# Kernel optimization log

Hardware: AMD Instinct MI355X
Metric: run time of the kernel (lower is better)

## Reference

```python
import jax, jax.numpy as jnp
import numpy as np

B, N, E, C, K, D, L, FC, IN, OUT = 2, 40000, 320000, 128, 64, 2, 4, 128, 3, 1


def _gelu(x):
    return jax.nn.gelu(x, approximate=False)  # torch F.gelu default = exact erf


def _compute_gradient(f, tgt, src, egw):
    # f: [B,C,N]; tgt,src: [B,E] int; egw: [B,E,D] -> returns [B, C*D, N]
    fT = f.transpose(0, 2, 1)  # [B,N,C]
    diff = jnp.take_along_axis(fT, src[..., None], axis=1) - jnp.take_along_axis(fT, tgt[..., None], axis=1)  # [B,E,C]
    msg = (diff[:, :, :, None] * egw[:, :, None, :]).reshape(fT.shape[0], tgt.shape[1], -1)  # [B,E,C*D], c outer / d inner
    g = jnp.zeros((fT.shape[0], fT.shape[1], msg.shape[-1]), f.dtype)
    g = g.at[jnp.arange(fT.shape[0])[:, None], tgt].add(msg)  # scatter_add over target nodes
    return g.transpose(0, 2, 1)


def _spectral(x, wc, ws, w0, bc, bs, b0, wbc, wbs, wb0):
    # x: [B,Cin,N]; wc/ws: [Cin,Cout,K]; w0: [Cin,Cout,1]; bases: [B,N,K] or [B,N,1]
    xc = jnp.einsum('bix,bxk->bik', x, wbc)
    xs = -jnp.einsum('bix,bxk->bik', x, wbs)
    x0 = jnp.einsum('bix,bxk->bik', x, wb0)
    fc = jnp.einsum('bik,iok->bok', xc, wc) - jnp.einsum('bik,iok->bok', xs, ws)
    fs = jnp.einsum('bik,iok->bok', xs, wc) + jnp.einsum('bik,iok->bok', xc, ws)
    f0 = jnp.einsum('bik,iok->bok', x0, w0)
    return (jnp.einsum('bok,bxk->box', f0, b0)
            + 2.0 * jnp.einsum('bok,bxk->box', fc, bc)
            - 2.0 * jnp.einsum('bok,bxk->box', fs, bs))


def _forward(x, node_mask, nodes, node_weights, edge_gradient_weights, modes,
             fc0_w, fc0_b, sp_wc, sp_ws, sp_w0, w_w, w_b, gw_w, gw_b,
             fc1_w, fc1_b, fc2_w, fc2_b, directed_edges):
    temp = jnp.einsum('bxd,kd->bxk', nodes, modes)
    bc = jnp.cos(temp) * node_mask
    bs = jnp.sin(temp) * node_mask
    b0 = node_mask
    wbc, wbs, wb0 = bc * node_weights, bs * node_weights, b0 * node_weights
    h = (x @ fc0_w + fc0_b).transpose(0, 2, 1)  # lift -> [B,C,N]
    tgt = directed_edges[..., 0]
    src = directed_edges[..., 1]
    nl = sp_wc.shape[0]
    for i in range(nl):
        x1 = _spectral(h, sp_wc[i], sp_ws[i], sp_w0[i], bc, bs, b0, wbc, wbs, wb0)
        x2 = jnp.einsum('oc,bcn->bon', w_w[i], h) + w_b[i][None, :, None]  # 1x1 conv
        # x3 is computed but NOT added, exactly matching the source (x = x1 + x2)
        x3 = jnp.einsum('oc,bcn->bon', gw_w[i],
                        jax.nn.soft_sign(_compute_gradient(h, tgt, src, edge_gradient_weights))) + gw_b[i][None, :, None]
        h = x1 + x2
        if i != nl - 1:
            h = _gelu(h)
    h = h.transpose(0, 2, 1)  # [B,N,C]
    h = _gelu(h @ fc1_w + fc1_b)
    return h @ fc2_w + fc2_b  # [B,N,OUT]


def setup_inputs() -> dict:
    key = jax.random.key(0)
    ks = jax.random.split(key, 16)
    scale = 1.0 / float(C * C)
    return {
        'x': jax.random.normal(ks[0], (B, N, IN), jnp.float32),
        'node_mask': jnp.ones((B, N, 1), jnp.float32),
        'nodes': jax.random.uniform(ks[1], (B, N, D), jnp.float32),
        'node_weights': jax.random.uniform(ks[2], (B, N, 1), jnp.float32) * (1.0 / N),
        'directed_edges': jax.random.randint(ks[3], (B, E, 2), 0, N, dtype=jnp.int32),
        'edge_gradient_weights': jax.random.normal(ks[4], (B, E, D), jnp.float32) * 0.1,
        'modes': jax.random.normal(ks[5], (K, D), jnp.float32) * 4.0,
        'fc0_w': jax.random.normal(ks[6], (IN, C), jnp.float32) * float(1.0 / np.sqrt(IN)),
        'fc0_b': jnp.zeros((C,), jnp.float32),
        'sp_wc': jax.random.uniform(ks[7], (L, C, C, K), jnp.float32) * scale,
        'sp_ws': jax.random.uniform(ks[8], (L, C, C, K), jnp.float32) * scale,
        'sp_w0': jax.random.uniform(ks[9], (L, C, C, 1), jnp.float32) * scale,
        'w_w': jax.random.normal(ks[10], (L, C, C), jnp.float32) * float(1.0 / np.sqrt(C)),
        'w_b': jnp.zeros((L, C), jnp.float32),
        'gw_w': jax.random.normal(ks[11], (L, C, D * C), jnp.float32) * float(1.0 / np.sqrt(D * C)),
        'gw_b': jnp.zeros((L, C), jnp.float32),
        'fc1_w': jax.random.normal(ks[12], (C, FC), jnp.float32) * float(1.0 / np.sqrt(C)),
        'fc1_b': jnp.zeros((FC,), jnp.float32),
        'fc2_w': jax.random.normal(ks[13], (FC, OUT), jnp.float32) * float(1.0 / np.sqrt(FC)),
        'fc2_b': jnp.zeros((OUT,), jnp.float32),
    }


def reference(x, node_mask, nodes, node_weights, directed_edges, edge_gradient_weights, modes,
              fc0_w, fc0_b, sp_wc, sp_ws, sp_w0, w_w, w_b, gw_w, gw_b,
              fc1_w, fc1_b, fc2_w, fc2_b):
    return _forward(x, node_mask, nodes, node_weights, edge_gradient_weights, modes,
                    fc0_w, fc0_b, sp_wc, sp_ws, sp_w0, w_w, w_b, gw_w, gw_b,
                    fc1_w, fc1_b, fc2_w, fc2_b, directed_edges)
```

## Files before the change

### kernel.cpp

```cpp
#include <hip/hip_runtime.h>
#include <math.h>

#define NN 40000
#define NP 40064
#define CC 128
#define KK 64
#define BATCH 2
#define NLAYER 4
#define FSPLITS 128
#define MODES 144
#define KTOT 256
#define NCH 626
#define NVCH 625

typedef __attribute__((ext_vector_type(8))) short bf16x8;
typedef __attribute__((ext_vector_type(4))) float f32x4;
typedef __attribute__((ext_vector_type(4))) unsigned short u16x4;
typedef __attribute__((ext_vector_type(8))) unsigned short u16x8;

__device__ __forceinline__ float gelu_exact(float x) {
    return 0.5f * x * (1.0f + erff(x * 0.70710678118654752f));
}
__device__ __forceinline__ unsigned short f2bf(float x) {
    unsigned int u = __float_as_uint(x);
    u += 0x7FFFu + ((u >> 16) & 1u);
    return (unsigned short)(u >> 16);
}
__device__ __forceinline__ float bf2f(unsigned short v) {
    return __uint_as_float(((unsigned int)v) << 16);
}

__global__ __launch_bounds__(512) void lift_fused(const float* __restrict__ x,
        const float* __restrict__ w, const float* __restrict__ bvec,
        const float* __restrict__ nodes, const float* __restrict__ mask,
        const float* __restrict__ wts, const float* __restrict__ modes,
        const float* __restrict__ fc1w, unsigned short* __restrict__ fc1t,
        unsigned short* __restrict__ Binv, float* __restrict__ maskp,
        float* __restrict__ warr, unsigned short* __restrict__ pxcs) {
    int s = blockIdx.x, b = blockIdx.y;
    int t = threadIdx.x, wv = t >> 6, l = t & 63, lo = l & 15, hi = l >> 4;
    if (b == 0 && s < 32) {
        int idx = s * 512 + t;
        int f = idx >> 7, c = idx & 127;
        fc1t[f * 128 + c] = f2bf(fc1w[c * 128 + f]);
    }
    __shared__ __align__(16) char lds[53504];
    char* Ts   = lds;
    char* Ts2  = lds + 16384;
    char* Wt   = lds + 32768;
    float* xl  = (float*)(lds + 51200);
    float* ndl = (float*)(lds + 51968);
    float* wl  = (float*)(lds + 52480);
    float* ml  = (float*)(lds + 52736);
    float* sm  = (float*)(lds + 52992);
    int c = t & 127, ng = t >> 7;
    float w0 = w[c], w1 = w[CC + c], w2 = w[2 * CC + c], bv = bvec[c];
    f32x4 accF[9];
    #pragma unroll
    for (int mt = 0; mt < 9; ++mt) accF[mt] = (f32x4){0.f, 0.f, 0.f, 0.f};
    if (t < 128) sm[t] = modes[t];
    if (t < 480) *(unsigned int*)(Wt + 129 * 128 + t * 4) = 0u;

    auto fetch = [&](int chunk) -> float {
        if (chunk >= NVCH) return 0.f;
        long base = (long)b * NN + chunk * 64;
        if (t < 192) return x[base * 3 + t];
        if (t < 320) return nodes[base * 2 + (t - 192)];
        if (t < 384) return wts[base + (t - 320)];
        if (t < 448) return mask[base + (t - 384)];
        return 0.f;
    };
    float pf = fetch(s);

    for (int chunk = s; chunk < NCH; chunk += FSPLITS) {
        int nbase = chunk * 64;
        __syncthreads();
        {
            if (t < 192)      xl[t] = pf;
            else if (t < 320) ndl[t - 192] = pf;
            else if (t < 384) wl[t - 320] = pf;
            else if (t < 448) ml[t - 384] = pf;
        }
        int nc = chunk + FSPLITS;
        if (nc < NCH) pf = fetch(nc);
        __syncthreads();
        {
            int n_ = t & 63, g = t >> 6;
            float nx = ndl[n_ * 2], ny = ndl[n_ * 2 + 1];
            float m = ml[n_];
            u16x8 cosr, sinr;
            #pragma unroll
            for (int j = 0; j < 8; ++j) {
                int k = g * 8 + j;
                float tv = nx * sm[2 * k] + ny * sm[2 * k + 1];
                float sv, cv;
                __sincosf(tv, &sv, &cv);
                unsigned short cb = f2bf(cv * m), sb = f2bf(sv * m);
                cosr[j] = cb; sinr[j] = sb;
                *(unsigned short*)(Wt + ((k * 128 + n_ * 2) ^ ((k & 7) << 4))) = cb;
                *(unsigned short*)(Wt + (((64 + k) * 128 + n_ * 2) ^ (((64 + k) & 7) << 4))) = sb;
            }
            char* brow = (char*)Binv + ((long)b * NP + nbase + n_) * 512 + g * 16;
            *(u16x8*)brow = cosr;
            *(u16x8*)(brow + 128) = sinr;
            if (t < 64) {
                *(unsigned short*)(Wt + 128 * 128 + n_ * 2) = f2bf(m);
                maskp[(long)b * NP + nbase + n_] = m;
                warr[(long)b * NP + nbase + n_] = wl[n_];
            }
        }
        {
            u16x8 hv0, hv1;
            #pragma unroll
            for (int j = 0; j < 16; ++j) {
                int n = ng * 16 + j;
                float h = bv + xl[n * 3] * w0 + xl[n * 3 + 1] * w1 + xl[n * 3 + 2] * w2;
                unsigned short hb = f2bf(h);
                unsigned short hwb = f2bf(h * wl[n]);
                if (j < 8) hv0[j] = hwb; else hv1[j - 8] = hwb;
                *(unsigned short*)(Ts + (((n << 8) + c * 2) ^ ((n & 7) << 4))) = hb;
            }
            int base2 = c * 128 + ng * 32;
            *(u16x8*)(Ts2 + (base2 ^ ((c & 7) << 4))) = hv0;
            *(u16x8*)(Ts2 + ((base2 + 16) ^ ((c & 7) << 4))) = hv1;
        }
        __syncthreads();
        char* Bdst = (char*)Binv + ((long)b * NP + nbase) * 512 + 256;
        #pragma unroll
        for (int pass = 0; pass < 2; ++pass) {
            int n = pass * 32 + (t >> 4), seg = t & 15;
            uint4 v = *(const uint4*)(Ts + (((n << 8) + (seg << 4)) ^ ((n & 7) << 4)));
            *(uint4*)(Bdst + (long)n * 512 + seg * 16) = v;
        }
        int ct = wv * 16;
        #pragma unroll
        for (int ks2 = 0; ks2 < 2; ++ks2) {
            int ar = ct + lo;
            bf16x8 a = *(const bf16x8*)(Ts2 + ((ar * 128 + ks2 * 64 + hi * 16) ^ ((ar & 7) << 4)));
            #pragma unroll
            for (int mt = 0; mt < 9; ++mt) {
                int mrow = mt * 16 + lo;
                bf16x8 bb = *(const bf16x8*)(Wt + ((mrow * 128 + ks2 * 64 + hi * 16) ^ ((mrow & 7) << 4)));
                accF[mt] = __builtin_amdgcn_mfma_f32_16x16x32_bf16(a, bb, accF[mt], 0, 0, 0);
            }
        }
    }
    unsigned short* pb = pxcs + ((long)s * BATCH + b) * CC * MODES;
    #pragma unroll
    for (int mt = 0; mt < 9; ++mt)
        #pragma unroll
        for (int r = 0; r < 4; ++r)
            pb[(long)(wv * 16 + hi * 4 + r) * MODES + mt * 16 + lo] = f2bf(accF[mt][r]);
}

__global__ __launch_bounds__(256) void reduce_kernel(const unsigned short* __restrict__ pxcs,
        float* __restrict__ xc, float* __restrict__ xs, float* __restrict__ x0) {
    int gid = blockIdx.x * 256 + threadIdx.x;
    int idx = gid >> 3, sg = gid & 7;
    float a = 0.f;
    #pragma unroll
    for (int j = 0; j < 16; ++j)
        a += bf2f(pxcs[(long)(sg * 16 + j) * (BATCH * CC * MODES) + idx]);
    a += __shfl_xor(a, 1); a += __shfl_xor(a, 2); a += __shfl_xor(a, 4);
    if (sg == 0) {
        int m = idx % MODES, bc_ = idx / MODES;
        if (m < 64)        xc[bc_ * KK + m] = a;
        else if (m < 128)  xs[bc_ * KK + m - 64] = a;
        else if (m == 128) x0[bc_] = a;
    }
}

__global__ __launch_bounds__(1024) void mix_kernel(const float* __restrict__ xc,
        const float* __restrict__ xs, const float* __restrict__ x0,
        const float* __restrict__ wc, const float* __restrict__ wsp,
        const float* __restrict__ w0, const float* __restrict__ ww,
        const float* __restrict__ wbias, unsigned short* __restrict__ A,
        float* __restrict__ f0a, float* __restrict__ wba, int layer) {
    int o = blockIdx.x, b = blockIdx.y;
    int k = threadIdx.x & 63, ig = threadIdx.x >> 6;
    const float* wcl = wc  + (long)layer * CC * CC * KK;
    const float* wsl = wsp + (long)layer * CC * CC * KK;
    float fc = 0.f, fs = 0.f;
    #pragma unroll
    for (int j = 0; j < 8; ++j) {
        int i = ig * 8 + j;
        float xci = xc[(b * CC + i) * KK + k];
        float xsi = xs[(b * CC + i) * KK + k];
        float wcv = wcl[((long)i * CC + o) * KK + k];
        float wsv = wsl[((long)i * CC + o) * KK + k];
        fc += xci * wcv + xsi * wsv;
        fs += xci * wsv - xsi * wcv;
    }
    __shared__ float rc[16][64], rs[16][64];
    rc[ig][k] = fc; rs[ig][k] = fs;
    __syncthreads();
    unsigned short* Ar = A + ((long)b * CC + o) * KTOT;
    if (ig == 0) {
        fc = 0.f; fs = 0.f;
        #pragma unroll
        for (int j = 0; j < 16; ++j) { fc += rc[j][k]; fs += rs[j][k]; }
        Ar[k]      = f2bf(2.f * fc);
        Ar[64 + k] = f2bf(-2.f * fs);
    } else if (ig == 1) {
        const float* wwl = ww + ((long)layer * CC + o) * CC;
        Ar[128 + k] = f2bf(wwl[k]);
        Ar[192 + k] = f2bf(wwl[64 + k]);
    } else if (ig == 2) {
        const float* w0l = w0 + (long)layer * CC * CC;
        float p = x0[b * CC + k] * w0l[(long)k * CC + o]
                + x0[b * CC + 64 + k] * w0l[(long)(64 + k) * CC + o];
        #pragma unroll
        for (int off = 32; off > 0; off >>= 1) p += __shfl_down(p, off, 64);
        if (k == 0) { f0a[b * CC + o] = p; wba[b * CC + o] = wbias[layer * CC + o]; }
    }
}

template <int DO_FWD, int DOGELU>
__global__ __launch_bounds__(512) void fused_inv(const unsigned short* __restrict__ Amat,
        unsigned short* Binv, const float* __restrict__ f0a, const float* __restrict__ wba,
        const float* __restrict__ maskp, const float* __restrict__ warr,
        unsigned short* __restrict__ pxcs) {
    int s = blockIdx.x, b = blockIdx.y;
    int t = threadIdx.x, wv = t >> 6, l = t & 63, lo = l & 15, hi = l >> 4;
    __shared__ __align__(16) char lds[51712];
    char* Btile = lds;
    char* Ts    = lds;
    char* Ts2   = lds + 16384;
    char* Wt    = lds + 32768;
    float* ml   = (float*)(lds + 51200);
    float* wl   = (float*)(lds + 51456);
    const unsigned short* Ab = Amat + (long)b * CC * KTOT;
    bf16x8 af[8];
    {
        const unsigned short* arow = Ab + (long)(wv * 16 + lo) * KTOT + hi * 8;
        #pragma unroll
        for (int ks = 0; ks < 8; ++ks) af[ks] = *(const bf16x8*)(arow + ks * 32);
    }
    int o0 = wv * 16 + hi * 4;
    f32x4 f0v = *(const f32x4*)(f0a + b * CC + o0);
    f32x4 wbv = *(const f32x4*)(wba + b * CC + o0);
    int swz = (lo & 7) << 4;
    f32x4 accF[9];
    #pragma unroll
    for (int mt = 0; mt < 9; ++mt) accF[mt] = (f32x4){0.f, 0.f, 0.f, 0.f};
    const char* Bbase = (const char*)Binv + (long)b * NP * 512;
    if (DO_FWD && t < 480) *(unsigned int*)(Wt + 129 * 128 + t * 4) = 0u;

    uint4 pB0 = {}, pB1 = {}, pB2 = {}, pB3 = {};
    float pmv = 0.f, pwv = 0.f;
    {
        const char* Bsrc = Bbase + (long)s * 64 * 512;
        pB0 = *(const uint4*)(Bsrc + 0 * 8192 + t * 16);
        pB1 = *(const uint4*)(Bsrc + 1 * 8192 + t * 16);
        pB2 = *(const uint4*)(Bsrc + 2 * 8192 + t * 16);
        pB3 = *(const uint4*)(Bsrc + 3 * 8192 + t * 16);
        if (t < 64) { pmv = maskp[(long)b * NP + s * 64 + t]; pwv = warr[(long)b * NP + s * 64 + t]; }
    }

    for (int chunk = s; chunk < NCH; chunk += FSPLITS) {
        int nbase = chunk * 64;
        __syncthreads();
        {
            int o = 0 * 8192 + t * 16; *(uint4*)(Btile + (o ^ (((o >> 9) & 7) << 4))) = pB0;
            o = 1 * 8192 + t * 16;     *(uint4*)(Btile + (o ^ (((o >> 9) & 7) << 4))) = pB1;
            o = 2 * 8192 + t * 16;     *(uint4*)(Btile + (o ^ (((o >> 9) & 7) << 4))) = pB2;
            o = 3 * 8192 + t * 16;     *(uint4*)(Btile + (o ^ (((o >> 9) & 7) << 4))) = pB3;
            if (t < 64) { ml[t] = pmv; wl[t] = pwv; }
        }
        int nc = chunk + FSPLITS;
        if (nc < NCH) {
            const char* Bsrc = Bbase + (long)nc * 64 * 512;
            pB0 = *(const uint4*)(Bsrc + 0 * 8192 + t * 16);
            pB1 = *(const uint4*)(Bsrc + 1 * 8192 + t * 16);
            pB2 = *(const uint4*)(Bsrc + 2 * 8192 + t * 16);
            pB3 = *(const uint4*)(Bsrc + 3 * 8192 + t * 16);
            if (t < 64) { pmv = maskp[(long)b * NP + nc * 64 + t]; pwv = warr[(long)b * NP + nc * 64 + t]; }
        }
        __syncthreads();
        if (DO_FWD) {
            int g = t >> 6, n_ = t & 63;
            int rkey = (n_ & 7) << 4;
            int raddr = n_ * 512 + g * 32;
            u16x8 r0 = *(const u16x8*)(Btile + (raddr ^ rkey));
            u16x8 r1 = *(const u16x8*)(Btile + ((raddr + 16) ^ rkey));
            #pragma unroll
            for (int i = 0; i < 8; ++i) {
                int mr = g * 16 + i;
                *(unsigned short*)(Wt + ((mr * 128 + n_ * 2) ^ ((mr & 7) << 4))) = r0[i];
            }
            #pragma unroll
            for (int i = 0; i < 8; ++i) {
                int mr = g * 16 + 8 + i;
                *(unsigned short*)(Wt + ((mr * 128 + n_ * 2) ^ ((mr & 7) << 4))) = r1[i];
            }
            if (t < 64) *(unsigned short*)(Wt + 128 * 128 + t * 2) = f2bf(ml[t]);
        }
        f32x4 acc[4];
        #pragma unroll
        for (int fn = 0; fn < 4; ++fn) acc[fn] = (f32x4){0.f, 0.f, 0.f, 0.f};
        #pragma unroll
        for (int ks = 0; ks < 8; ++ks) {
            #pragma unroll
            for (int fn = 0; fn < 4; ++fn) {
                int boff = ((fn * 16 + lo) << 9) + (ks << 6) + (hi << 4);
                bf16x8 bb = *(const bf16x8*)(Btile + (boff ^ swz));
                acc[fn] = __builtin_amdgcn_mfma_f32_16x16x32_bf16(af[ks], bb, acc[fn], 0, 0, 0);
            }
        }
        __syncthreads();
        #pragma unroll
        for (int fn = 0; fn < 4; ++fn) {
            int n = fn * 16 + lo;
            float mv = ml[n];
            u16x4 pk;
            #pragma unroll
            for (int r = 0; r < 4; ++r) {
                float v = acc[fn][r] + f0v[r] * mv + wbv[r];
                if (DOGELU) v = gelu_exact(v);
                pk[r] = f2bf(v);
                if (DO_FWD)
                    *(unsigned short*)(Ts2 + (((o0 + r) * 128 + n * 2) ^ (((o0 + r) & 7) << 4))) = f2bf(v * wl[n]);
            }
            *(u16x4*)(Ts + (((n << 8) + (o0 << 1)) ^ ((n & 7) << 4))) = pk;
        }
        __syncthreads();
        char* Bdst = (char*)Binv + ((long)b * NP + nbase) * 512 + 256;
        #pragma unroll
        for (int pass = 0; pass < 2; ++pass) {
            int n = pass * 32 + (t >> 4), seg = t & 15;
            uint4 v = *(const uint4*)(Ts + (((n << 8) + (seg << 4)) ^ ((n & 7) << 4)));
            *(uint4*)(Bdst + (long)n * 512 + seg * 16) = v;
        }
        if (DO_FWD) {
            int ct = wv * 16;
            #pragma unroll
            for (int ks2 = 0; ks2 < 2; ++ks2) {
                int ar = ct + lo;
                bf16x8 a = *(const bf16x8*)(Ts2 + ((ar * 128 + ks2 * 64 + hi * 16) ^ ((ar & 7) << 4)));
                #pragma unroll
                for (int mt = 0; mt < 9; ++mt) {
                    int mrow = mt * 16 + lo;
                    bf16x8 bb = *(const bf16x8*)(Wt + ((mrow * 128 + ks2 * 64 + hi * 16) ^ ((mrow & 7) << 4)));
                    accF[mt] = __builtin_amdgcn_mfma_f32_16x16x32_bf16(a, bb, accF[mt], 0, 0, 0);
                }
            }
        }
    }
    if (DO_FWD) {
        unsigned short* pb = pxcs + ((long)s * BATCH + b) * CC * MODES;
        #pragma unroll
        for (int mt = 0; mt < 9; ++mt)
            #pragma unroll
            for (int r = 0; r < 4; ++r)
                pb[(long)(wv * 16 + hi * 4 + r) * MODES + mt * 16 + lo] = f2bf(accF[mt][r]);
    }
}

__global__ __launch_bounds__(256) void head_mfma(const unsigned short* __restrict__ Binv,
        const unsigned short* __restrict__ fc1t, const float* __restrict__ b1,
        const float* __restrict__ fc2, const float* __restrict__ b2, float* __restrict__ out) {
    int t = threadIdx.x, wv = t >> 6, l = t & 63, lo = l & 15, hi = l >> 4;
    int b = blockIdx.y;
    int nb = (blockIdx.x * 4 + wv) * 16;
    const unsigned short* Arow = Binv + ((long)b * NP + nb + lo) * KTOT + 128 + hi * 8;
    f32x4 acc[8];
    #pragma unroll
    for (int ft = 0; ft < 8; ++ft) acc[ft] = (f32x4){0.f, 0.f, 0.f, 0.f};
    #pragma unroll
    for (int ks = 0; ks < 4; ++ks) {
        bf16x8 a = *(const bf16x8*)(Arow + ks * 32);
        #pragma unroll
        for (int ft = 0; ft < 8; ++ft) {
            bf16x8 bv = *(const bf16x8*)(fc1t + (ft * 16 + lo) * 128 + ks * 32 + hi * 8);
            acc[ft] = __builtin_amdgcn_mfma_f32_16x16x32_bf16(a, bv, acc[ft], 0, 0, 0);
        }
    }
    float s[4] = {0.f, 0.f, 0.f, 0.f};
    #pragma unroll
    for (int ft = 0; ft < 8; ++ft) {
        int f = ft * 16 + lo;
        float b1f = b1[f], f2f = fc2[f];
        #pragma unroll
        for (int r = 0; r < 4; ++r) s[r] += gelu_exact(acc[ft][r] + b1f) * f2f;
    }
    float b2v = b2[0];
    #pragma unroll
    for (int r = 0; r < 4; ++r) {
        float v = s[r];
        v += __shfl_xor(v, 1); v += __shfl_xor(v, 2);
        v += __shfl_xor(v, 4); v += __shfl_xor(v, 8);
        if (lo == 0) out[(long)b * NN + nb + hi * 4 + r] = v + b2v;
    }
}

extern "C" void kernel_launch(void* const* d_in, const int* in_sizes, int n_in,
                              void* d_out, int out_size, void* d_ws, size_t ws_size,
                              hipStream_t stream) {
    const float* x     = (const float*)d_in[0];
    const float* mask  = (const float*)d_in[1];
    const float* nodes = (const float*)d_in[2];
    const float* wts   = (const float*)d_in[3];
    const float* modes = (const float*)d_in[6];
    const float* fc0w  = (const float*)d_in[7];
    const float* fc0b  = (const float*)d_in[8];
    const float* spwc  = (const float*)d_in[9];
    const float* spws  = (const float*)d_in[10];
    const float* spw0  = (const float*)d_in[11];
    const float* ww    = (const float*)d_in[12];
    const float* wb    = (const float*)d_in[13];
    const float* fc1w  = (const float*)d_in[16];
    const float* fc1b  = (const float*)d_in[17];
    const float* fc2w  = (const float*)d_in[18];
    const float* fc2b  = (const float*)d_in[19];

    char* p = (char*)d_ws;
    auto alloc = [&](size_t bytes) { char* r = p; p += (bytes + 255) & ~255UL; return r; };
    unsigned short* Binv = (unsigned short*)alloc((size_t)BATCH * NP * KTOT * 2);
    unsigned short* Amat = (unsigned short*)alloc((size_t)BATCH * CC * KTOT * 2);
    unsigned short* fc1t = (unsigned short*)alloc((size_t)CC * 128 * 2);
    unsigned short* pxcs = (unsigned short*)alloc((size_t)FSPLITS * BATCH * CC * MODES * 2);
    float* xcb  = (float*)alloc((size_t)BATCH * CC * KK * 4);
    float* xsb  = (float*)alloc((size_t)BATCH * CC * KK * 4);
    float* x0b  = (float*)alloc((size_t)BATCH * CC * 4);
    float* f0a  = (float*)alloc((size_t)BATCH * CC * 4);
    float* wba  = (float*)alloc((size_t)BATCH * CC * 4);
    float* maskp = (float*)alloc((size_t)BATCH * NP * 4);
    float* warr  = (float*)alloc((size_t)BATCH * NP * 4);

    lift_fused<<<dim3(FSPLITS, BATCH), 512, 0, stream>>>(x, fc0w, fc0b, nodes, mask, wts,
                                                         modes, fc1w, fc1t, Binv, maskp, warr, pxcs);

    for (int l = 0; l < NLAYER; ++l) {
        reduce_kernel<<<(8 * BATCH * CC * MODES) / 256, 256, 0, stream>>>(pxcs, xcb, xsb, x0b);
        mix_kernel<<<dim3(CC, BATCH), 1024, 0, stream>>>(xcb, xsb, x0b, spwc, spws, spw0,
                                                         ww, wb, Amat, f0a, wba, l);
        if (l < NLAYER - 1)
            fused_inv<1, 1><<<dim3(FSPLITS, BATCH), 512, 0, stream>>>(
                Amat, Binv, f0a, wba, maskp, warr, pxcs);
        else
            fused_inv<0, 0><<<dim3(FSPLITS, BATCH), 512, 0, stream>>>(
                Amat, Binv, f0a, wba, maskp, warr, pxcs);
    }
    head_mfma<<<dim3(NN / 64, BATCH), 256, 0, stream>>>(Binv, fc1t, fc1b, fc2w, fc2b, (float*)d_out);
}
```

Baseline: 191.8 us.

## Double-buffer B tiles via direct global-to-LDS loads and drop barriers

Replaces the register-staged prefetch of the B tile with asynchronous global_load_lds copies into two alternating LDS buffers. The XOR swizzle is applied to the source address, so the tile still lands swizzled in LDS. Ts, Ts2 and Wt move to their own LDS regions instead of aliasing the B tile. That removes two of the per-iteration __syncthreads; the barrier before the write-out becomes an lgkmcnt wait plus s_barrier. Mask and weight values are now read straight from global memory into registers rather than staged through LDS. The cost is that LDS use grows to about 117 KB per block, which lowers occupancy, and the kernel now depends on the async LDS loads completing before the closing barrier.

```diff
diff --git a/kernel.cpp b/kernel.cpp
--- a/kernel.cpp
+++ b/kernel.cpp
@@ -28,6 +28,15 @@
 }
 __device__ __forceinline__ float bf2f(unsigned short v) {
     return __uint_as_float(((unsigned int)v) << 16);
+}
+__device__ __forceinline__ void bar_lgkm() {
+    asm volatile("s_waitcnt lgkmcnt(0)" ::: "memory");
+    __builtin_amdgcn_s_barrier();
+}
+__device__ __forceinline__ void gload16(const void* g, void* l) {
+    __builtin_amdgcn_global_load_lds(
+        (const __attribute__((address_space(1))) void*)g,
+        (__attribute__((address_space(3))) void*)l, 16, 0, 0);
 }
 
 __global__ __launch_bounds__(512) void lift_fused(const float* __restrict__ x,
@@ -222,13 +231,10 @@
         unsigned short* __restrict__ pxcs) {
     int s = blockIdx.x, b = blockIdx.y;
     int t = threadIdx.x, wv = t >> 6, l = t & 63, lo = l & 15, hi = l >> 4;
-    __shared__ __align__(16) char lds[51712];
-    char* Btile = lds;
-    char* Ts    = lds;
-    char* Ts2   = lds + 16384;
-    char* Wt    = lds + 32768;
-    float* ml   = (float*)(lds + 51200);
-    float* wl   = (float*)(lds + 51456);
+    __shared__ __align__(16) char lds[117248];
+    char* Ts  = lds + 65536;
+    char* Ts2 = lds + 81920;
+    char* Wt  = lds + 98304;
     const unsigned short* Ab = Amat + (long)b * CC * KTOT;
     bf16x8 af[8];
     {
@@ -246,43 +252,37 @@
     const char* Bbase = (const char*)Binv + (long)b * NP * 512;
     if (DO_FWD && t < 480) *(unsigned int*)(Wt + 129 * 128 + t * 4) = 0u;
 
-    uint4 pB0 = {}, pB1 = {}, pB2 = {}, pB3 = {};
-    float pmv = 0.f, pwv = 0.f;
-    {
-        const char* Bsrc = Bbase + (long)s * 64 * 512;
-        pB0 = *(const uint4*)(Bsrc + 0 * 8192 + t * 16);
-        pB1 = *(const uint4*)(Bsrc + 1 * 8192 + t * 16);
-        pB2 = *(const uint4*)(Bsrc + 2 * 8192 + t * 16);
-        pB3 = *(const uint4*)(Bsrc + 3 * 8192 + t * 16);
-        if (t < 64) { pmv = maskp[(long)b * NP + s * 64 + t]; pwv = warr[(long)b * NP + s * 64 + t]; }
-    }
-
-    for (int chunk = s; chunk < NCH; chunk += FSPLITS) {
+    auto stage = [&](int chunk, char* Bt) {
+        const char* Bsrc = Bbase + (long)chunk * 64 * 512;
+        #pragma unroll
+        for (int j = 0; j < 4; ++j) {
+            int off = j * 8192 + t * 16;
+            int soff = off ^ (((off >> 9) & 7) << 4);
+            gload16(Bsrc + soff, Bt + off);
+        }
+    };
+    stage(s, lds);
+    __syncthreads();
+
+    int iter = 0;
+    for (int chunk = s; chunk < NCH; chunk += FSPLITS, ++iter) {
+        char* BtP = lds + (iter & 1) * 32768;
+        char* BtQ = lds + ((iter & 1) ^ 1) * 32768;
         int nbase = chunk * 64;
-        __syncthreads();
-        {
-            int o = 0 * 8192 + t * 16; *(uint4*)(Btile + (o ^ (((o >> 9) & 7) << 4))) = pB0;
-            o = 1 * 8192 + t * 16;     *(uint4*)(Btile + (o ^ (((o >> 9) & 7) << 4))) = pB1;
-            o = 2 * 8192 + t * 16;     *(uint4*)(Btile + (o ^ (((o >> 9) & 7) << 4))) = pB2;
-            o = 3 * 8192 + t * 16;     *(uint4*)(Btile + (o ^ (((o >> 9) & 7) << 4))) = pB3;
-            if (t < 64) { ml[t] = pmv; wl[t] = pwv; }
-        }
         int nc = chunk + FSPLITS;
-        if (nc < NCH) {
-            const char* Bsrc = Bbase + (long)nc * 64 * 512;
-            pB0 = *(const uint4*)(Bsrc + 0 * 8192 + t * 16);
-            pB1 = *(const uint4*)(Bsrc + 1 * 8192 + t * 16);
-            pB2 = *(const uint4*)(Bsrc + 2 * 8192 + t * 16);
-            pB3 = *(const uint4*)(Bsrc + 3 * 8192 + t * 16);
-            if (t < 64) { pmv = maskp[(long)b * NP + nc * 64 + t]; pwv = warr[(long)b * NP + nc * 64 + t]; }
-        }
-        __syncthreads();
+        if (nc < NCH) stage(nc, BtQ);
+        float mvv[4], wvv[4];
+        #pragma unroll
+        for (int fn = 0; fn < 4; ++fn) {
+            mvv[fn] = maskp[(long)b * NP + nbase + fn * 16 + lo];
+            wvv[fn] = DO_FWD ? warr[(long)b * NP + nbase + fn * 16 + lo] : 0.f;
+        }
         if (DO_FWD) {
             int g = t >> 6, n_ = t & 63;
             int rkey = (n_ & 7) << 4;
             int raddr = n_ * 512 + g * 32;
-            u16x8 r0 = *(const u16x8*)(Btile + (raddr ^ rkey));
-            u16x8 r1 = *(const u16x8*)(Btile + ((raddr + 16) ^ rkey));
+            u16x8 r0 = *(const u16x8*)(BtP + (raddr ^ rkey));
+            u16x8 r1 = *(const u16x8*)(BtP + ((raddr + 16) ^ rkey));
             #pragma unroll
             for (int i = 0; i < 8; ++i) {
                 int mr = g * 16 + i;
@@ -293,7 +293,8 @@
                 int mr = g * 16 + 8 + i;
                 *(unsigned short*)(Wt + ((mr * 128 + n_ * 2) ^ ((mr & 7) << 4))) = r1[i];
             }
-            if (t < 64) *(unsigned short*)(Wt + 128 * 128 + t * 2) = f2bf(ml[t]);
+            if (t < 64)
+                *(unsigned short*)(Wt + 128 * 128 + t * 2) = f2bf(maskp[(long)b * NP + nbase + t]);
         }
         f32x4 acc[4];
         #pragma unroll
@@ -303,27 +304,25 @@
             #pragma unroll
             for (int fn = 0; fn < 4; ++fn) {
                 int boff = ((fn * 16 + lo) << 9) + (ks << 6) + (hi << 4);
-                bf16x8 bb = *(const bf16x8*)(Btile + (boff ^ swz));
+                bf16x8 bb = *(const bf16x8*)(BtP + (boff ^ swz));
                 acc[fn] = __builtin_amdgcn_mfma_f32_16x16x32_bf16(af[ks], bb, acc[fn], 0, 0, 0);
             }
         }
-        __syncthreads();
         #pragma unroll
         for (int fn = 0; fn < 4; ++fn) {
             int n = fn * 16 + lo;
-            float mv = ml[n];
             u16x4 pk;
             #pragma unroll
             for (int r = 0; r < 4; ++r) {
-                float v = acc[fn][r] + f0v[r] * mv + wbv[r];
+                float v = acc[fn][r] + f0v[r] * mvv[fn] + wbv[r];
                 if (DOGELU) v = gelu_exact(v);
                 pk[r] = f2bf(v);
                 if (DO_FWD)
-                    *(unsigned short*)(Ts2 + (((o0 + r) * 128 + n * 2) ^ (((o0 + r) & 7) << 4))) = f2bf(v * wl[n]);
+                    *(unsigned short*)(Ts2 + (((o0 + r) * 128 + n * 2) ^ (((o0 + r) & 7) << 4))) = f2bf(v * wvv[fn]);
             }
             *(u16x4*)(Ts + (((n << 8) + (o0 << 1)) ^ ((n & 7) << 4))) = pk;
         }
-        __syncthreads();
+        bar_lgkm();
         char* Bdst = (char*)Binv + ((long)b * NP + nbase) * 512 + 256;
         #pragma unroll
         for (int pass = 0; pass < 2; ++pass) {
@@ -345,6 +344,7 @@
                 }
             }
         }
+        __syncthreads();
     }
     if (DO_FWD) {
         unsigned short* pb = pxcs + ((long)s * BATCH + b) * CC * MODES;
```

Result: slower. 196.2 us (+2.3%).
